# Kernel optimization log

Measured on AMD Instinct MI355X. Metric: run time of the kernel, lower is better.

Reference implementation:

```python
import jax, jax.numpy as jnp
import numpy as np

BITS = 8
EPS = 1e-08


def _scalar_quantize_maxabs(x, scale, bits, eps):
    # clamp(round(x / scale), -qmax, qmax) with a fixed (precomputed) scalar scale
    qmax = float(2 ** (bits - 1) - 1)
    s = jnp.maximum(scale, eps)
    return jnp.clip(jnp.round(x / s), -qmax, qmax)


def setup_inputs() -> dict:
    key = jax.random.key(0)
    k1, k2, k3 = jax.random.split(key, 3)
    B, S, D_in, D_out = 4, 2048, 2048, 2048
    hidden_states = jax.random.normal(k1, (B, S, D_in), dtype=jnp.float32)
    # weight_quantized holds low-bit integer values stored as float (as produced by the quantizer)
    qmax = float(2 ** (BITS - 1) - 1)
    weight_quantized = jnp.round(
        jnp.clip(jax.random.normal(k2, (D_in, D_out), dtype=jnp.float32) * (qmax / 3.0), -qmax, qmax)
    )
    x_scale = jnp.asarray(0.05, dtype=jnp.float32)
    bias = jax.random.normal(k3, (D_out,), dtype=jnp.float32)
    return {
        "hidden_states": hidden_states,
        "weight_quantized": weight_quantized,
        "x_scale": x_scale,
        "bias": bias,
    }


def reference(hidden_states, weight_quantized, x_scale, bias) -> jnp.ndarray:
    original_shape = hidden_states.shape[:-1]
    input_dim = hidden_states.shape[-1]
    x_flat = hidden_states.reshape(-1, input_dim)  # [B*S, D_in]
    x_q = _scalar_quantize_maxabs(x_flat, x_scale.reshape(()), BITS, EPS)
    out = x_q.astype(weight_quantized.dtype) @ weight_quantized  # [B*S, D_out]
    out = out + bias.astype(out.dtype)[None, :]
    return out.astype(hidden_states.dtype).reshape(*original_shape, weight_quantized.shape[1])
```

## Files before the change

### kernel.cpp

```cpp
#include <hip/hip_runtime.h>
#include <cstdint>
#include <cstddef>

#define MDIM 8192
#define NDIM 2048
#define KDIM 2048

constexpr int BM = 256, BN = 256, BK = 64;
constexpr int NT = KDIM / BK;
constexpr int NBUF = 4;

typedef int v4i __attribute__((ext_vector_type(4)));

__device__ __forceinline__ void async_ld16(const void* g, void* l) {
    __builtin_amdgcn_global_load_lds(
        (const __attribute__((address_space(1))) int*)g,
        (__attribute__((address_space(3))) int*)l,
        16, 0, 0);
}

__device__ __forceinline__ uint32_t q8(float x, float inv) {
    float q = fminf(fmaxf(rintf(x * inv), -127.f), 127.f);
    return (uint32_t)((int)q) & 0xffu;
}

#define XBLOCKS (MDIM * KDIM / 4 / 256)

__global__ void quant_kernel(const float4* __restrict__ x, uint32_t* __restrict__ xq,
                             const float* __restrict__ scale_p,
                             const float* __restrict__ w, uint32_t* __restrict__ wt) {
    __shared__ uint32_t t[64][17];
    const int tid = threadIdx.x;

    if (blockIdx.x < XBLOCKS) {
        int i = blockIdx.x * 256 + tid;
        float inv = 1.0f / fmaxf(scale_p[0], 1e-8f);
        float4 v = x[i];
        xq[i] = q8(v.x, inv) | (q8(v.y, inv) << 8) | (q8(v.z, inv) << 16) | (q8(v.w, inv) << 24);
        return;
    }

    const int bid = blockIdx.x - XBLOCKS;
    const int k0 = (bid >> 5) * 64;
    const int n0 = (bid & 31) * 64;
    const int rr  = tid >> 4;
    const int c4  = (tid & 15) * 4;
#pragma unroll
    for (int p = 0; p < 4; ++p) {
        int r = rr + p * 16;
        float4 v = *(const float4*)&w[(size_t)(k0 + r) * NDIM + n0 + c4];
        uint32_t pk = (uint32_t)((int)rintf(v.x) & 0xff)
                    | ((uint32_t)((int)rintf(v.y) & 0xff) << 8)
                    | ((uint32_t)((int)rintf(v.z) & 0xff) << 16)
                    | ((uint32_t)((int)rintf(v.w) & 0xff) << 24);
        t[r][c4 >> 2] = pk;
    }
    __syncthreads();
#pragma unroll
    for (int p = 0; p < 4; ++p) {
        int c = rr + p * 16;
        uint32_t o = 0;
#pragma unroll
        for (int j = 0; j < 4; ++j) {
            uint32_t b = (t[c4 + j][c >> 2] >> ((c & 3) * 8)) & 0xffu;
            o |= b << (j * 8);
        }
        wt[((size_t)(n0 + c) * KDIM + k0 + c4) >> 2] = o;
    }
}

__global__ __launch_bounds__(512, 2)
void gemm_i8_kernel(const int8_t* __restrict__ A,
                    const int8_t* __restrict__ Bt,
                    const float* __restrict__ bias,
                    float* __restrict__ C) {
    __shared__ alignas(16) int8_t lA[NBUF][BM * BK];
    __shared__ alignas(16) int8_t lB[NBUF][BN * BK];

    const int tid  = threadIdx.x;
    const int lane = tid & 63;
    const int wave = tid >> 6;
    const int wm   = wave & 1;
    const int wn   = wave >> 1;

    const int bidlin = blockIdx.y * gridDim.x + blockIdx.x;
    const int swz    = (bidlin & 7) * 32 + (bidlin >> 3);
    const int m0     = (swz >> 3) * BM;
    const int n0     = (swz & 7) * BN;

    const int srow = lane >> 2;
    const int schk = (lane & 3) ^ ((srow >> 1) & 3);
    const int8_t* gA = A  + (size_t)(m0 + wave * 32 + srow) * KDIM + schk * 16;
    const int8_t* gB = Bt + (size_t)(n0 + wave * 32 + srow) * KDIM + schk * 16;
    const int lwo = wave * 2048;

    const int quad = lane >> 4;
    const int lr   = lane & 15;
    const int fchk = (quad ^ ((lr >> 1) & 3)) * 16;
    const int aoff = (wm * 128 + lr) * BK + fchk;
    const int boff = (wn * 64 + lr) * BK + fchk;

    v4i acc[8][4];
#pragma unroll
    for (int i = 0; i < 8; ++i)
#pragma unroll
        for (int j = 0; j < 4; ++j)
            acc[i][j] = (v4i){0, 0, 0, 0};

#define STAGE(buf, kof)                                                        \
    do {                                                                       \
        async_ld16(gA + (kof), &lA[buf][lwo]);                                 \
        async_ld16(gA + (kof) + (size_t)16 * KDIM, &lA[buf][lwo + 1024]);      \
        async_ld16(gB + (kof), &lB[buf][lwo]);                                 \
        async_ld16(gB + (kof) + (size_t)16 * KDIM, &lB[buf][lwo + 1024]);      \
    } while (0)

#define COMPUTE(buf)                                                           \
    do {                                                                       \
        v4i bf[4];                                                             \
        _Pragma("unroll")                                                      \
        for (int j = 0; j < 4; ++j)                                            \
            bf[j] = *(const v4i*)&lB[buf][boff + j * 1024];                    \
        __builtin_amdgcn_s_setprio(1);                                         \
        _Pragma("unroll")                                                      \
        for (int i = 0; i < 8; ++i) {                                          \
            v4i af = *(const v4i*)&lA[buf][aoff + i * 1024];                   \
            _Pragma("unroll")                                                  \
            for (int j = 0; j < 4; ++j)                                        \
                acc[i][j] = __builtin_amdgcn_mfma_i32_16x16x64_i8(             \
                    af, bf[j], acc[i][j], 0, 0, 0);                            \
        }                                                                      \
        __builtin_amdgcn_s_setprio(0);                                        \
    } while (0)

#define WAITBAR(n)                                                             \
    do {                                                                       \
        asm volatile("s_waitcnt vmcnt(" #n ")" ::: "memory");                  \
        __builtin_amdgcn_s_barrier();                                          \
        asm volatile("" ::: "memory");                                         \
    } while (0)

    STAGE(0, 0);
    STAGE(1, BK);
    STAGE(2, 2 * BK);

    int kof = 3 * BK;
    for (int t = 0; t < NT - 3; ++t) {
        WAITBAR(8);
        STAGE((t + 3) & 3, kof);
        kof += BK;
        COMPUTE(t & 3);
    }
    WAITBAR(8);
    COMPUTE((NT - 3) & 3);
    WAITBAR(4);
    COMPUTE((NT - 2) & 3);
    WAITBAR(0);
    COMPUTE((NT - 1) & 3);

#undef STAGE
#undef COMPUTE
#undef WAITBAR

    const int crow = m0 + wm * 128 + quad * 4;
    const int ccol = n0 + wn * 64 + lr;
    float bj[4];
#pragma unroll
    for (int j = 0; j < 4; ++j) bj[j] = bias[ccol + j * 16];
#pragma unroll
    for (int i = 0; i < 8; ++i)
#pragma unroll
        for (int j = 0; j < 4; ++j)
#pragma unroll
            for (int r = 0; r < 4; ++r)
                C[(size_t)(crow + i * 16 + r) * NDIM + (ccol + j * 16)] = (float)acc[i][j][r] + bj[j];
}

extern "C" void kernel_launch(void* const* d_in, const int* in_sizes, int n_in,
                              void* d_out, int out_size, void* d_ws, size_t ws_size,
                              hipStream_t stream) {
    const float* x    = (const float*)d_in[0];
    const float* w    = (const float*)d_in[1];
    const float* xs   = (const float*)d_in[2];
    const float* bias = (const float*)d_in[3];
    float* out = (float*)d_out;

    int8_t* xq = (int8_t*)d_ws;
    int8_t* wt = xq + (size_t)MDIM * KDIM;

    quant_kernel<<<XBLOCKS + (KDIM / 64) * (NDIM / 64), 256, 0, stream>>>(
        (const float4*)x, (uint32_t*)xq, xs, w, (uint32_t*)wt);
    gemm_i8_kernel<<<dim3(NDIM / BN, MDIM / BM), 512, 0, stream>>>(xq, wt, bias, out);
}
```

Measured before the change: 171.6 us.

## Split each K-tile into four barrier-synchronized phases interleaving loads with MFMAs

Restructures the GEMM main loop into four phases per K tile. Each phase reads two A fragments, issues one of the four async global-to-LDS loads for a future stage, then runs eight MFMAs between two workgroup barriers, in the style of the 'ping-pong' schedules used in AMD's hipBLASLt kernels. The aim is to spread memory issue across the compute and keep waves in lockstep so LDS reads and MFMAs overlap better. The cost is eight barriers per K tile instead of one, plus tighter synchronisation that could stall waves.

```diff
diff --git a/kernel.cpp b/kernel.cpp
--- a/kernel.cpp
+++ b/kernel.cpp
@@ -107,7 +107,7 @@
         for (int j = 0; j < 4; ++j)
             acc[i][j] = (v4i){0, 0, 0, 0};
 
-#define STAGE(buf, kof)                                                        \
+#define STAGE_ALL(buf, kof)                                                    \
     do {                                                                       \
         async_ld16(gA + (kof), &lA[buf][lwo]);                                 \
         async_ld16(gA + (kof) + (size_t)16 * KDIM, &lA[buf][lwo + 1024]);      \
@@ -115,52 +115,78 @@
         async_ld16(gB + (kof) + (size_t)16 * KDIM, &lB[buf][lwo + 1024]);      \
     } while (0)
 
-#define COMPUTE(buf)                                                           \
-    do {                                                                       \
-        v4i bf[4];                                                             \
-        _Pragma("unroll")                                                      \
-        for (int j = 0; j < 4; ++j)                                            \
-            bf[j] = *(const v4i*)&lB[buf][boff + j * 1024];                    \
+#define PHASE(tb, p, STAGE_STMT, TAIL_STMT)                                    \
+    do {                                                                       \
+        if ((p) == 0) {                                                        \
+            _Pragma("unroll")                                                  \
+            for (int j = 0; j < 4; ++j)                                        \
+                bf[j] = *(const v4i*)&lB[tb][boff + j * 1024];                 \
+        }                                                                      \
+        v4i af0 = *(const v4i*)&lA[tb][aoff + (2 * (p)) * 1024];               \
+        v4i af1 = *(const v4i*)&lA[tb][aoff + (2 * (p) + 1) * 1024];           \
+        STAGE_STMT;                                                            \
+        asm volatile("" ::: "memory");                                         \
+        __builtin_amdgcn_s_barrier();                                          \
+        asm volatile("s_waitcnt lgkmcnt(0)" ::: "memory");                     \
         __builtin_amdgcn_s_setprio(1);                                         \
         _Pragma("unroll")                                                      \
-        for (int i = 0; i < 8; ++i) {                                          \
-            v4i af = *(const v4i*)&lA[buf][aoff + i * 1024];                   \
-            _Pragma("unroll")                                                  \
-            for (int j = 0; j < 4; ++j)                                        \
-                acc[i][j] = __builtin_amdgcn_mfma_i32_16x16x64_i8(             \
-                    af, bf[j], acc[i][j], 0, 0, 0);                            \
+        for (int j = 0; j < 4; ++j) {                                          \
+            acc[2 * (p)][j] = __builtin_amdgcn_mfma_i32_16x16x64_i8(           \
+                af0, bf[j], acc[2 * (p)][j], 0, 0, 0);                         \
+            acc[2 * (p) + 1][j] = __builtin_amdgcn_mfma_i32_16x16x64_i8(       \
+                af1, bf[j], acc[2 * (p) + 1][j], 0, 0, 0);                     \
         }                                                                      \
         __builtin_amdgcn_s_setprio(0);                                        \
-    } while (0)
-
-#define WAITBAR(n)                                                             \
-    do {                                                                       \
-        asm volatile("s_waitcnt vmcnt(" #n ")" ::: "memory");                  \
+        TAIL_STMT;                                                             \
+        asm volatile("" ::: "memory");                                         \
         __builtin_amdgcn_s_barrier();                                          \
-        asm volatile("" ::: "memory");                                         \
-    } while (0)
-
-    STAGE(0, 0);
-    STAGE(1, BK);
-    STAGE(2, 2 * BK);
+    } while (0)
+
+#define NOSTAGE ((void)0)
+#define VM(n) asm volatile("s_waitcnt vmcnt(" #n ")" ::: "memory")
+
+#define KTILE_MAIN(tb, sb, kof)                                                \
+    do {                                                                       \
+        v4i bf[4];                                                             \
+        PHASE(tb, 0, async_ld16(gA + (kof), &lA[sb][lwo]), NOSTAGE);           \
+        PHASE(tb, 1, async_ld16(gA + (kof) + (size_t)16 * KDIM,                \
+                                &lA[sb][lwo + 1024]), NOSTAGE);                \
+        PHASE(tb, 2, async_ld16(gB + (kof), &lB[sb][lwo]), NOSTAGE);           \
+        PHASE(tb, 3, async_ld16(gB + (kof) + (size_t)16 * KDIM,               \
+                                &lB[sb][lwo + 1024]), VM(8));                  \
+    } while (0)
+
+#define KTILE_TAIL(tb, TAILW)                                                  \
+    do {                                                                       \
+        v4i bf[4];                                                             \
+        PHASE(tb, 0, NOSTAGE, NOSTAGE);                                        \
+        PHASE(tb, 1, NOSTAGE, NOSTAGE);                                        \
+        PHASE(tb, 2, NOSTAGE, NOSTAGE);                                        \
+        PHASE(tb, 3, NOSTAGE, TAILW);                                          \
+    } while (0)
+
+    STAGE_ALL(0, 0);
+    STAGE_ALL(1, BK);
+    STAGE_ALL(2, 2 * BK);
+    VM(8);
+    asm volatile("" ::: "memory");
+    __builtin_amdgcn_s_barrier();
 
     int kof = 3 * BK;
     for (int t = 0; t < NT - 3; ++t) {
-        WAITBAR(8);
-        STAGE((t + 3) & 3, kof);
+        KTILE_MAIN(t & 3, (t + 3) & 3, kof);
         kof += BK;
-        COMPUTE(t & 3);
-    }
-    WAITBAR(8);
-    COMPUTE((NT - 3) & 3);
-    WAITBAR(4);
-    COMPUTE((NT - 2) & 3);
-    WAITBAR(0);
-    COMPUTE((NT - 1) & 3);
-
-#undef STAGE
-#undef COMPUTE
-#undef WAITBAR
+    }
+    KTILE_TAIL((NT - 3) & 3, VM(4));
+    KTILE_TAIL((NT - 2) & 3, VM(0));
+    KTILE_TAIL((NT - 1) & 3, NOSTAGE);
+
+#undef STAGE_ALL
+#undef PHASE
+#undef NOSTAGE
+#undef VM
+#undef KTILE_MAIN
+#undef KTILE_TAIL
 
     const int crow = m0 + wm * 128 + quad * 4;
     const int ccol = n0 + wn * 64 + lr;
```

Result: no change. 171.9 us (+0.2%).
